# Optimization experiments

Hardware: AMD Instinct MI355X
Metric: run time of the kernel (lower is better)

## Reference

```python
import jax, jax.numpy as jnp
import numpy as np

B, K, D = 1024, 262144, 64

def setup_inputs() -> dict:
    key = jax.random.key(0)
    k1, k2 = jax.random.split(key)
    query_vec = jax.random.normal(k1, (B, D), dtype=jnp.float32)
    memory = jax.random.normal(k2, (K, D), dtype=jnp.float32)
    return {"query_vec": query_vec, "memory": memory, "topk": 5}

def reference(query_vec, memory, topk):
    # sim: [B, K] similarity against the full memory bank
    sim = jnp.einsum('bd,kd->bk', query_vec, memory)
    # indices of top-k most similar bank rows: [B, topk]
    _, topk_idx = jax.lax.top_k(sim, topk)
    # gather rows: [B, topk, D]
    return memory[topk_idx]
```

## Files before the change

kernel.cpp:

```cpp
#include <hip/hip_runtime.h>
#include <stdint.h>

typedef unsigned long long u64;
typedef __attribute__((ext_vector_type(8))) short short8;
typedef __attribute__((ext_vector_type(4))) float f32x4;

#define KROWS  262144
#define DDIM   64
#define NQ     1024
#define NC     128
#define CHUNK  (KROWS / NC)
#define SUB    128
#define NSUB   (CHUNK / SUB)
#define KSTRIDE 8
#define BIAS   128.0f
#define SIMMASK 0xFFFFF800u

__device__ __forceinline__ uint32_t ord32(float f) {
    uint32_t u = __float_as_uint(f);
    return (u & 0x80000000u) ? ~u : (u | 0x80000000u);
}
__device__ __forceinline__ uint32_t med3u(uint32_t a, uint32_t b, uint32_t c) {
    uint32_t d;
    asm("v_med3_u32 %0, %1, %2, %3" : "=v"(d) : "v"(a), "v"(b), "v"(c));
    return d;
}
__device__ __forceinline__ void fold5(uint32_t (&t)[5], uint32_t k) {
    uint32_t n4 = med3u(t[3], t[4], k);
    uint32_t n3 = med3u(t[2], t[3], k);
    uint32_t n2 = med3u(t[1], t[2], k);
    uint32_t n1 = med3u(t[0], t[1], k);
    t[0] = t[0] > k ? t[0] : k;
    t[1] = n1; t[2] = n2; t[3] = n3; t[4] = n4;
}
__device__ __forceinline__ uint32_t bf16rne(float f) {
    uint32_t u = __float_as_uint(f);
    return (u + 0x7fffu + ((u >> 16) & 1u)) >> 16;
}
__device__ __forceinline__ uint32_t pack2(float a, float b) {
    return bf16rne(a) | (bf16rne(b) << 16);
}
__device__ __forceinline__ void gload_lds16(const void* g, void* l) {
    __builtin_amdgcn_global_load_lds(
        (const __attribute__((address_space(1))) uint32_t*)g,
        (__attribute__((address_space(3))) uint32_t*)l, 16, 0, 0);
}

__global__ __launch_bounds__(256) void conv(const float* __restrict__ Mf,
                                            uint16_t* __restrict__ Mb) {
    const int stride = gridDim.x * 256;
    const float4* src = (const float4*)Mf;
    uint4* dst = (uint4*)Mb;
    for (int e = blockIdx.x * 256 + threadIdx.x; e < (KROWS * DDIM / 8); e += stride) {
        const float4 a = src[2 * e], b = src[2 * e + 1];
        uint4 o;
        o.x = pack2(a.x, a.y); o.y = pack2(a.z, a.w);
        o.z = pack2(b.x, b.y); o.w = pack2(b.z, b.w);
        dst[e] = o;
    }
}

__global__ __launch_bounds__(512, 4) void p1(const float* __restrict__ Qg,
                                             const uint16_t* __restrict__ Mb,
                                             uint32_t* __restrict__ wsK) {
    __shared__ __align__(16) uint16_t stage[2 * 8192];
    const int t = threadIdx.x;
    const int lane = t & 63;
    const int w = t >> 6;
    const int quad = lane >> 4;
    const int m = lane & 15;
    const int qcol = blockIdx.x;
    const int chunk = blockIdx.y;
    const int qBase = qcol * 256 + w * 32;
    const int rowChunk = chunk * CHUNK;

    short8 afr[2][2];
    #pragma unroll
    for (int qt = 0; qt < 2; ++qt)
        #pragma unroll
        for (int kh = 0; kh < 2; ++kh) {
            const float* qp = Qg + (size_t)(qBase + qt * 16 + m) * DDIM + quad * 8 + kh * 32;
            const float4 f0 = ((const float4*)qp)[0];
            const float4 f1 = ((const float4*)qp)[1];
            short8 a;
            a[0] = (short)bf16rne(f0.x); a[1] = (short)bf16rne(f0.y);
            a[2] = (short)bf16rne(f0.z); a[3] = (short)bf16rne(f0.w);
            a[4] = (short)bf16rne(f1.x); a[5] = (short)bf16rne(f1.y);
            a[6] = (short)bf16rne(f1.z); a[7] = (short)bf16rne(f1.w);
            afr[qt][kh] = a;
        }
    const f32x4 bias = {BIAS, BIAS, BIAS, BIAS};

    uint32_t top[8][5];
    #pragma unroll
    for (int li = 0; li < 8; ++li)
        #pragma unroll
        for (int s = 0; s < 5; ++s) top[li][s] = 0u;

    auto stage_sub = [&](int sb, int buf) {
        const uint16_t* src = Mb + (size_t)(rowChunk + sb * SUB) * DDIM;
        #pragma unroll
        for (int i = 0; i < 2; ++i) {
            const int slotBase = w * 128 + i * 64;
            const int slot = slotBase + lane;
            const int row = slot >> 3, c = slot & 7;
            const int g = row * 8 + (c ^ (row & 7));
            gload_lds16(src + (size_t)g * 8, stage + buf * 8192 + slotBase * 8);
        }
    };

    stage_sub(0, 0);
    for (int sb = 0; sb < NSUB; ++sb) {
        __syncthreads();
        if (sb + 1 < NSUB) stage_sub(sb + 1, (sb + 1) & 1);
        const uint16_t* bufp = stage + (sb & 1) * 8192;
        const uint32_t pb = (uint32_t)m + (uint32_t)sb * 128u;
        #pragma unroll
        for (int rt = 0; rt < 8; ++rt) {
            const int r = rt * 16 + m;
            const short8 b0 = *(const short8*)(bufp + r * 64 + ((quad       ^ (m & 7)) * 8));
            const short8 b1 = *(const short8*)(bufp + r * 64 + (((quad + 4) ^ (m & 7)) * 8));
            f32x4 c0, c1;
            c0 = __builtin_amdgcn_mfma_f32_16x16x32_bf16(afr[0][0], b0, bias, 0, 0, 0);
            c0 = __builtin_amdgcn_mfma_f32_16x16x32_bf16(afr[0][1], b1, c0,   0, 0, 0);
            c1 = __builtin_amdgcn_mfma_f32_16x16x32_bf16(afr[1][0], b0, bias, 0, 0, 0);
            c1 = __builtin_amdgcn_mfma_f32_16x16x32_bf16(afr[1][1], b1, c1,   0, 0, 0);
            const uint32_t posm = pb + (uint32_t)(rt * 16);
            #pragma unroll
            for (int reg = 0; reg < 4; ++reg) {
                fold5(top[reg],     (__float_as_uint(c0[reg]) & SIMMASK) | posm);
                fold5(top[4 + reg], (__float_as_uint(c1[reg]) & SIMMASK) | posm);
            }
        }
    }

    #pragma unroll
    for (int d = 1; d <= 8; d <<= 1) {
        #pragma unroll
        for (int li = 0; li < 8; ++li) {
            uint32_t rm[5];
            #pragma unroll
            for (int s = 0; s < 5; ++s) rm[s] = __shfl_xor(top[li][s], d, 64);
            #pragma unroll
            for (int s = 0; s < 5; ++s) fold5(top[li], rm[s]);
        }
    }

    if (m == 0) {
        #pragma unroll
        for (int li = 0; li < 8; ++li) {
            const int q = qBase + (li >> 2) * 16 + quad * 4 + (li & 3);
            uint32_t* p = wsK + ((size_t)chunk * NQ + (size_t)q) * KSTRIDE;
            uint4 v4; v4.x = top[li][0]; v4.y = top[li][1];
            v4.z = top[li][2]; v4.w = top[li][3];
            *(uint4*)p = v4;
            p[4] = top[li][4];
        }
    }
}

__global__ __launch_bounds__(64) void p2(const float* __restrict__ Qg,
                                         const float* __restrict__ Mf,
                                         const uint32_t* __restrict__ wsK,
                                         float* __restrict__ out) {
    const int Q = blockIdx.x;
    const int lane = threadIdx.x;
    u64 mk[10];
    #pragma unroll
    for (int i = 0; i < 10; ++i) {
        const int flat = i * 64 + lane;
        const int c = flat / 5, s = flat - c * 5;
        const uint32_t k = wsK[((size_t)c * NQ + (size_t)Q) * KSTRIDE + s];
        const uint32_t grow = (uint32_t)c * (uint32_t)CHUNK + (k & 2047u);
        mk[i] = ((u64)k << 32) | (u64)grow;
    }
    uint32_t idxs[16];
    #pragma unroll
    for (int it = 0; it < 16; ++it) {
        u64 wk = mk[0];
        #pragma unroll
        for (int i2 = 1; i2 < 10; ++i2) wk = mk[i2] > wk ? mk[i2] : wk;
        #pragma unroll
        for (int off = 32; off >= 1; off >>= 1) {
            const u64 o = __shfl_xor(wk, off, 64);
            wk = o > wk ? o : wk;
        }
        #pragma unroll
        for (int i2 = 0; i2 < 10; ++i2) if (mk[i2] == wk) mk[i2] = 0;
        idxs[it] = (uint32_t)wk;
    }
    const float qv = Qg[(size_t)Q * DDIM + lane];
    float v[16];
    #pragma unroll
    for (int j = 0; j < 16; ++j) v[j] = Mf[(size_t)idxs[j] * DDIM + lane];
    u64 rk[16];
    #pragma unroll
    for (int j = 0; j < 16; ++j) {
        float p = qv * v[j];
        #pragma unroll
        for (int off = 32; off >= 1; off >>= 1) p += __shfl_xor(p, off, 64);
        rk[j] = ((u64)ord32(p) << 32) | (u64)(~idxs[j]);
    }
    #pragma unroll
    for (int it = 0; it < 5; ++it) {
        u64 best = rk[0];
        #pragma unroll
        for (int j = 1; j < 16; ++j) best = rk[j] > best ? rk[j] : best;
        float o = 0.f;
        #pragma unroll
        for (int j = 0; j < 16; ++j) o = (rk[j] == best) ? v[j] : o;
        out[((size_t)Q * 5 + it) * DDIM + lane] = o;
        #pragma unroll
        for (int j = 0; j < 16; ++j) rk[j] = (rk[j] == best) ? 0ull : rk[j];
    }
}

extern "C" void kernel_launch(void* const* d_in, const int* in_sizes, int n_in,
                              void* d_out, int out_size, void* d_ws, size_t ws_size,
                              hipStream_t stream) {
    const float* Qg = (const float*)d_in[0];
    const float* Mf = (const float*)d_in[1];
    float* out = (float*)d_out;
    uint32_t* wsK = (uint32_t*)d_ws;
    uint16_t* Mb = (uint16_t*)((char*)d_ws + (4u << 20));

    conv<<<2048, 256, 0, stream>>>(Mf, Mb);
    p1<<<dim3(4, NC), 512, 0, stream>>>(Qg, Mb, wsK);
    p2<<<NQ, 64, 0, stream>>>(Qg, Mf, wsK, out);
}
```

Baseline: 190.8 us.

## Track per-lane top-2 over smaller chunks instead of top-5 in similarity scan

Doubles the number of memory chunks and has each lane keep only a top-2 running list with cheap min/max updates instead of a med3-based top-5 insert. The cross-lane merge builds a top-4 per chunk and query, and p2 reads 4 candidates from each of 256 chunks. Occupancy is raised by increasing the launch-bounds minimum blocks. This cuts per-element selection ALU cost in the hot MFMA loop. The trade-off is that a query whose true top-5 has three or more hits in one lane's strided subset could lose a candidate, and the packed position field now has fewer bits.

```diff
diff --git a/kernel.cpp b/kernel.cpp
--- a/kernel.cpp
+++ b/kernel.cpp
@@ -8,30 +8,30 @@
 #define KROWS  262144
 #define DDIM   64
 #define NQ     1024
-#define NC     128
+#define NC     256
 #define CHUNK  (KROWS / NC)
 #define SUB    128
 #define NSUB   (CHUNK / SUB)
-#define KSTRIDE 8
+#define KC_PER 4
 #define BIAS   128.0f
-#define SIMMASK 0xFFFFF800u
+#define SIMMASK 0xFFFFFC00u
 
 __device__ __forceinline__ uint32_t ord32(float f) {
     uint32_t u = __float_as_uint(f);
     return (u & 0x80000000u) ? ~u : (u | 0x80000000u);
 }
-__device__ __forceinline__ uint32_t med3u(uint32_t a, uint32_t b, uint32_t c) {
-    uint32_t d;
-    asm("v_med3_u32 %0, %1, %2, %3" : "=v"(d) : "v"(a), "v"(b), "v"(c));
-    return d;
-}
-__device__ __forceinline__ void fold5(uint32_t (&t)[5], uint32_t k) {
-    uint32_t n4 = med3u(t[3], t[4], k);
-    uint32_t n3 = med3u(t[2], t[3], k);
-    uint32_t n2 = med3u(t[1], t[2], k);
-    uint32_t n1 = med3u(t[0], t[1], k);
-    t[0] = t[0] > k ? t[0] : k;
-    t[1] = n1; t[2] = n2; t[3] = n3; t[4] = n4;
+__device__ __forceinline__ uint32_t maxu(uint32_t a, uint32_t b) { return a > b ? a : b; }
+__device__ __forceinline__ uint32_t minu(uint32_t a, uint32_t b) { return a < b ? a : b; }
+__device__ __forceinline__ void fold2(uint32_t& t0, uint32_t& t1, uint32_t k) {
+    t1 = maxu(t1, minu(t0, k));
+    t0 = maxu(t0, k);
+}
+__device__ __forceinline__ void fold4(uint32_t (&t)[4], uint32_t k) {
+    uint32_t n1 = maxu(t[1], minu(t[0], k));
+    uint32_t n2 = maxu(t[2], minu(t[1], k));
+    uint32_t n3 = maxu(t[3], minu(t[2], k));
+    t[0] = maxu(t[0], k);
+    t[1] = n1; t[2] = n2; t[3] = n3;
 }
 __device__ __forceinline__ uint32_t bf16rne(float f) {
     uint32_t u = __float_as_uint(f);
@@ -60,7 +60,7 @@
     }
 }
 
-__global__ __launch_bounds__(512, 4) void p1(const float* __restrict__ Qg,
+__global__ __launch_bounds__(512, 8) void p1(const float* __restrict__ Qg,
                                              const uint16_t* __restrict__ Mb,
                                              uint32_t* __restrict__ wsK) {
     __shared__ __align__(16) uint16_t stage[2 * 8192];
@@ -91,11 +91,9 @@
         }
     const f32x4 bias = {BIAS, BIAS, BIAS, BIAS};
 
-    uint32_t top[8][5];
-    #pragma unroll
-    for (int li = 0; li < 8; ++li)
-        #pragma unroll
-        for (int s = 0; s < 5; ++s) top[li][s] = 0u;
+    uint32_t tA[8], tB[8];
+    #pragma unroll
+    for (int li = 0; li < 8; ++li) { tA[li] = 0u; tB[li] = 0u; }
 
     auto stage_sub = [&](int sb, int buf) {
         const uint16_t* src = Mb + (size_t)(rowChunk + sb * SUB) * DDIM;
@@ -128,21 +126,29 @@
             const uint32_t posm = pb + (uint32_t)(rt * 16);
             #pragma unroll
             for (int reg = 0; reg < 4; ++reg) {
-                fold5(top[reg],     (__float_as_uint(c0[reg]) & SIMMASK) | posm);
-                fold5(top[4 + reg], (__float_as_uint(c1[reg]) & SIMMASK) | posm);
+                fold2(tA[reg],     tB[reg],     (__float_as_uint(c0[reg]) & SIMMASK) | posm);
+                fold2(tA[4 + reg], tB[4 + reg], (__float_as_uint(c1[reg]) & SIMMASK) | posm);
             }
         }
     }
 
+    uint32_t fl[8][4];
+    #pragma unroll
+    for (int li = 0; li < 8; ++li) {
+        fl[li][0] = tA[li]; fl[li][1] = tB[li]; fl[li][2] = 0u; fl[li][3] = 0u;
+    }
     #pragma unroll
     for (int d = 1; d <= 8; d <<= 1) {
+        const int nv = (d == 1) ? 2 : 4;
         #pragma unroll
         for (int li = 0; li < 8; ++li) {
-            uint32_t rm[5];
+            uint32_t rm[4];
             #pragma unroll
-            for (int s = 0; s < 5; ++s) rm[s] = __shfl_xor(top[li][s], d, 64);
+            for (int s = 0; s < 4; ++s)
+                if (s < nv) rm[s] = __shfl_xor(fl[li][s], d, 64);
             #pragma unroll
-            for (int s = 0; s < 5; ++s) fold5(top[li], rm[s]);
+            for (int s = 0; s < 4; ++s)
+                if (s < nv) fold4(fl[li], rm[s]);
         }
     }
 
@@ -150,11 +156,9 @@
         #pragma unroll
         for (int li = 0; li < 8; ++li) {
             const int q = qBase + (li >> 2) * 16 + quad * 4 + (li & 3);
-            uint32_t* p = wsK + ((size_t)chunk * NQ + (size_t)q) * KSTRIDE;
-            uint4 v4; v4.x = top[li][0]; v4.y = top[li][1];
-            v4.z = top[li][2]; v4.w = top[li][3];
-            *(uint4*)p = v4;
-            p[4] = top[li][4];
+            uint4 v4; v4.x = fl[li][0]; v4.y = fl[li][1];
+            v4.z = fl[li][2]; v4.w = fl[li][3];
+            *(uint4*)(wsK + ((size_t)chunk * NQ + (size_t)q) * KC_PER) = v4;
         }
     }
 }
@@ -165,29 +169,31 @@
                                          float* __restrict__ out) {
     const int Q = blockIdx.x;
     const int lane = threadIdx.x;
-    u64 mk[10];
-    #pragma unroll
-    for (int i = 0; i < 10; ++i) {
-        const int flat = i * 64 + lane;
-        const int c = flat / 5, s = flat - c * 5;
-        const uint32_t k = wsK[((size_t)c * NQ + (size_t)Q) * KSTRIDE + s];
-        const uint32_t grow = (uint32_t)c * (uint32_t)CHUNK + (k & 2047u);
-        mk[i] = ((u64)k << 32) | (u64)grow;
+    u64 mk[16];
+    #pragma unroll
+    for (int i = 0; i < 4; ++i) {
+        const int c = i * 64 + lane;
+        const uint4 k4 = *(const uint4*)(wsK + ((size_t)c * NQ + (size_t)Q) * KC_PER);
+        const uint32_t cb = (uint32_t)c * (uint32_t)CHUNK;
+        mk[i * 4 + 0] = ((u64)k4.x << 32) | (u64)(cb + (k4.x & 1023u));
+        mk[i * 4 + 1] = ((u64)k4.y << 32) | (u64)(cb + (k4.y & 1023u));
+        mk[i * 4 + 2] = ((u64)k4.z << 32) | (u64)(cb + (k4.z & 1023u));
+        mk[i * 4 + 3] = ((u64)k4.w << 32) | (u64)(cb + (k4.w & 1023u));
     }
     uint32_t idxs[16];
     #pragma unroll
     for (int it = 0; it < 16; ++it) {
         u64 wk = mk[0];
         #pragma unroll
-        for (int i2 = 1; i2 < 10; ++i2) wk = mk[i2] > wk ? mk[i2] : wk;
+        for (int i2 = 1; i2 < 16; ++i2) wk = mk[i2] > wk ? mk[i2] : wk;
         #pragma unroll
         for (int off = 32; off >= 1; off >>= 1) {
             const u64 o = __shfl_xor(wk, off, 64);
             wk = o > wk ? o : wk;
         }
         #pragma unroll
-        for (int i2 = 0; i2 < 10; ++i2) if (mk[i2] == wk) mk[i2] = 0;
-        idxs[it] = (uint32_t)wk;
+        for (int i2 = 0; i2 < 16; ++i2) if (mk[i2] == wk) mk[i2] = 0;
+        idxs[it] = (uint32_t)wk & (KROWS - 1u);
     }
     const float qv = Qg[(size_t)Q * DDIM + lane];
     float v[16];
```

Result: slower. 283.9 us (+48.8%).
